# Kernel tuning notes

Measured on AMD Instinct MI355X. Metric: run time of the kernel, lower is better.

Reference implementation:

```python
import jax, jax.numpy as jnp
import numpy as np

N_NODES = 20000


def _agg(feat, src, dst):
    # copy_u + sum: for each edge, message = feat[src]; sum at dst over in-edges.
    # feat: [N, F], src/dst: [E] int32 -> [N, F]
    msgs = feat[src]  # [E, F]
    return jax.ops.segment_sum(msgs, dst, num_segments=N_NODES)


def setup_inputs() -> dict:
    key = jax.random.key(0)
    k1, k2, k3, k4, k5, k6, k7 = jax.random.split(key, 7)
    B, N, E = 4, N_NODES, 320000
    in_f, hid, out_f = 128, 256, 128
    features = jax.random.normal(k1, (B, N, in_f), dtype=jnp.float32)
    src = jax.random.randint(k2, (B, E), 0, N, dtype=jnp.int32)
    dst = jax.random.randint(k3, (B, E), 0, N, dtype=jnp.int32)
    s1 = 1.0 / np.sqrt(in_f)
    s2 = 1.0 / np.sqrt(hid)
    W1 = jax.random.uniform(k4, (in_f, hid), jnp.float32, -s1, s1)
    b1 = jax.random.uniform(k5, (hid,), jnp.float32, -s1, s1)
    W2 = jax.random.uniform(k6, (hid, out_f), jnp.float32, -s2, s2)
    b2 = jax.random.uniform(k7, (out_f,), jnp.float32, -s2, s2)
    return {"features": features, "src": src, "dst": dst,
            "W1": W1, "b1": b1, "W2": W2, "b2": b2}


def reference(features, src, dst, W1, b1, W2, b2):
    # vmap over the batch of graphs (replaces the per-graph Python loop)
    agg = jax.vmap(_agg)  # [B,N,F] -> [B,N,F]
    h = agg(features, src, dst)            # conv1 aggregation
    h = jnp.einsum('bnf,fh->bnh', h, W1) + b1  # conv1 linear
    h = jax.nn.relu(h)
    h = agg(h, src, dst)                   # conv2 aggregation
    out = jnp.einsum('bnh,ho->bno', h, W2) + b2  # conv2 linear
    return out
```

## Files before the change

kernel.cpp:

```cpp
#include <hip/hip_runtime.h>

#define NN 20000
#define NHALF 10000
#define NCH 16
#define SB 32
#define NBIN 625

typedef __attribute__((ext_vector_type(8))) __bf16 bf16x8;
typedef __attribute__((ext_vector_type(8))) unsigned short ushort8;
typedef __attribute__((ext_vector_type(4))) float f32x4;

__device__ __forceinline__ unsigned short f2bf(float f) {
    unsigned u = __builtin_bit_cast(unsigned, f);
    u += 0x7fff + ((u >> 16) & 1);
    return (unsigned short)(u >> 16);
}
__device__ __forceinline__ float bf2f(unsigned short h) {
    unsigned u = ((unsigned)h) << 16;
    return __builtin_bit_cast(float, u);
}


__global__ void k_tobf(const float* __restrict__ in, unsigned short* __restrict__ outp,
                       long n8) {
    long i = (long)blockIdx.x * 256 + threadIdx.x;
    if (i >= n8) return;
    const float4* s = (const float4*)(in + i * 8);
    float4 v0 = s[0], v1 = s[1];
    ushort8 r;
    r[0] = f2bf(v0.x); r[1] = f2bf(v0.y); r[2] = f2bf(v0.z); r[3] = f2bf(v0.w);
    r[4] = f2bf(v1.x); r[5] = f2bf(v1.y); r[6] = f2bf(v1.z); r[7] = f2bf(v1.w);
    *(ushort8*)(outp + i * 8) = r;
}


__global__ void k_hist(const int* __restrict__ dst, long dst_bs,
                       int* __restrict__ histc, int E, int ec) {
    int c = blockIdx.x, h = blockIdx.y, b = blockIdx.z;
    __shared__ int hist[NHALF];
    for (int i = threadIdx.x; i < NHALF; i += 1024) hist[i] = 0;
    __syncthreads();
    const int* d = dst + (size_t)b * dst_bs;
    int e0 = c * ec, e1 = min(e0 + ec, E);
    for (int e = e0 + threadIdx.x; e < e1; e += 1024) {
        int dd = d[e];
        if ((dd >= NHALF) == (h != 0)) atomicAdd(&hist[dd - h * NHALF], 1);
    }
    __syncthreads();
    int* out = histc + ((size_t)b * NCH + c) * NN + h * NHALF;
    for (int i = threadIdx.x; i < NHALF; i += 1024) out[i] = hist[i];
}


__global__ void k_scan2a(const int* __restrict__ histc,
                         int* __restrict__ offs, long off_bs,
                         int* __restrict__ chunkbase, int* __restrict__ btot) {
    int blk = blockIdx.x, b = blockIdx.z;
    const int* hc = histc + (size_t)b * NCH * NN;
    int* cb = chunkbase + (size_t)b * NCH * NN;
    int i = blk * NBIN + threadIdx.x;
    __shared__ int sums[1024];
    int hv[NCH];
    int s = 0;
    if (threadIdx.x < NBIN) {
#pragma unroll
        for (int c = 0; c < NCH; c++) { hv[c] = hc[c * NN + i]; s += hv[c]; }
    }
    sums[threadIdx.x] = (threadIdx.x < NBIN) ? s : 0;
    __syncthreads();
    for (int d2 = 1; d2 < 1024; d2 <<= 1) {
        int x = (threadIdx.x >= d2) ? sums[threadIdx.x - d2] : 0;
        __syncthreads();
        sums[threadIdx.x] += x;
        __syncthreads();
    }
    if (threadIdx.x == 1023) btot[b * 64 + blk] = sums[1023];
    if (threadIdx.x < NBIN) {
        int run = sums[threadIdx.x] - s;
        offs[(size_t)b * off_bs + i] = run;
#pragma unroll
        for (int c = 0; c < NCH; c++) { cb[c * NN + i] = run; run += hv[c]; }
    }
}


__global__ void k_scan2b(int* __restrict__ offs, long off_bs,
                         const int* __restrict__ btot, int* __restrict__ boff, int n) {
    int b = blockIdx.z;
    __shared__ int bo[SB + 1];
    int t = threadIdx.x;
    if (t == 0) {
        int run = 0;
        for (int k = 0; k < SB; k++) { bo[k] = run; run += btot[b * 64 + k]; }
        bo[SB] = run;
    }
    __syncthreads();
    if (t < SB) boff[b * 64 + t] = bo[t];
    if (t == 0) offs[(size_t)b * off_bs + n] = bo[SB];
    for (int i = t; i < n; i += 1024)
        offs[(size_t)b * off_bs + i] += bo[i / NBIN];
}


__global__ void k_fill2(const int* __restrict__ src, long src_bs,
                        const int* __restrict__ dst, long dst_bs,
                        const int* __restrict__ chunkbase,
                        const int* __restrict__ boff,
                        unsigned short* __restrict__ elist, long el_bs,
                        int E, int ec) {
    int c = blockIdx.x, h = blockIdx.y, b = blockIdx.z;
    __shared__ int cur[NHALF];
    __shared__ int bo[16];
    if (threadIdx.x < 16) bo[threadIdx.x] = boff[b * 64 + h * 16 + threadIdx.x];
    __syncthreads();
    const int* cb = chunkbase + ((size_t)b * NCH + c) * NN + h * NHALF;
    for (int i = threadIdx.x; i < NHALF; i += 1024)
        cur[i] = cb[i] + bo[i / NBIN];
    __syncthreads();
    const int* dp = dst + (size_t)b * dst_bs;
    const int* sp = src + (size_t)b * src_bs;
    unsigned short* el = elist + (size_t)b * el_bs;
    int e0 = c * ec, e1 = min(e0 + ec, E);
    for (int e = e0 + threadIdx.x; e < e1; e += 1024) {
        int dd = dp[e];
        if ((dd >= NHALF) == (h != 0)) {
            int p = atomicAdd(&cur[dd - h * NHALF], 1);
            el[p] = (unsigned short)sp[e];
        }
    }
}


template <bool BFOUT>
__global__ void k_agg(const unsigned short* __restrict__ feat, long feat_bs,
                      const int* __restrict__ offs, long off_bs,
                      const unsigned short* __restrict__ elist, long el_bs,
                      const float* __restrict__ bias,
                      void* __restrict__ o1,
                      long out_bs, int N, int nb, int nbx) {
    int gid = blockIdx.x;
    int xcd = gid & 7;
    int b = xcd % nb;
    int grp = xcd / nb;
    int pass = grp & 1;
    int sub = grp >> 1;
    int xh = (8 / nb) >> 1;
    int nbk = (gid >> 3) * xh + sub;
    if (nbk >= nbx) return;
    int g = threadIdx.x >> 3;
    int lane = threadIdx.x & 7;
    int n = nbk * 32 + g;
    if (n >= N) return;
    int col0 = pass * 64 + lane * 8;
    const unsigned short* fp = feat + (size_t)b * feat_bs + col0;
    const int* off = offs + (size_t)b * off_bs;
    const unsigned short* el = elist + (size_t)b * el_bs;
    int lo = off[n], hi = off[n + 1];
    float a0[8] = {}, a1[8] = {}, a2[8] = {}, a3[8] = {};
    auto acc = [&](float* a, ushort8 v) {
#pragma unroll
        for (int i = 0; i < 8; i++) a[i] += bf2f(v[i]);
    };
    int e = lo;
    for (; e < hi && (e & 3); e++)
        acc(a0, *(const ushort8*)&fp[(size_t)el[e] * 128]);
    for (; e + 4 <= hi; e += 4) {
        ushort4 idx = *(const ushort4*)&el[e];
        ushort8 v0 = *(const ushort8*)&fp[(size_t)idx.x * 128];
        ushort8 v1 = *(const ushort8*)&fp[(size_t)idx.y * 128];
        ushort8 v2 = *(const ushort8*)&fp[(size_t)idx.z * 128];
        ushort8 v3 = *(const ushort8*)&fp[(size_t)idx.w * 128];
        acc(a0, v0); acc(a1, v1); acc(a2, v2); acc(a3, v3);
    }
    for (; e < hi; e++)
        acc(a0, *(const ushort8*)&fp[(size_t)el[e] * 128]);
    float r[8];
#pragma unroll
    for (int i = 0; i < 8; i++) r[i] = (a0[i] + a1[i]) + (a2[i] + a3[i]);
    size_t oi = (size_t)b * out_bs + (size_t)n * 128 + col0;
    if (BFOUT) {
        ushort8 qh;
#pragma unroll
        for (int i = 0; i < 8; i++) qh[i] = f2bf(r[i]);
        *(ushort8*)((unsigned short*)o1 + oi) = qh;
    } else {
        float* op = (float*)o1 + oi;
        const float* bp = bias + col0;
#pragma unroll
        for (int i = 0; i < 8; i++) r[i] += bp[i];
        *(float4*)(op) = make_float4(r[0], r[1], r[2], r[3]);
        *(float4*)(op + 4) = make_float4(r[4], r[5], r[6], r[7]);
    }
}


__global__ void k_prep_w(const float* __restrict__ W1, const float* __restrict__ W2,
                         unsigned short* __restrict__ Wt1, unsigned short* __restrict__ Wt2) {
    int i = blockIdx.x * 256 + threadIdx.x;
    if (i < 128 * 256) {
        {
            int k = i / 256, n = i % 256;
            Wt1[n * 128 + k] = f2bf(W1[i]);
        }
        {
            int k = i / 128, n = i % 128;
            Wt2[n * 256 + k] = f2bf(W2[i]);
        }
    }
}


__launch_bounds__(256, 2)
__global__ void k_mlp(const unsigned short* __restrict__ A1, long A_bs,
                      const unsigned short* __restrict__ Wt1,
                      const unsigned short* __restrict__ Wt2,
                      const float* __restrict__ b1,
                      unsigned short* __restrict__ H2b, long C_bs,
                      int M, int ntiles) {
    __shared__ unsigned short HH[16 * 256];
    __shared__ unsigned short H2S[16 * 128];
    char* HHc = (char*)HH;
    char* H2c = (char*)H2S;
    int b = blockIdx.z;
    int w = threadIdx.x >> 6, lane = threadIdx.x & 63;
    int colg = lane & 15, kg = lane >> 4;

    bf16x8 w1f[4][4];
#pragma unroll
    for (int c = 0; c < 4; c++) {
        const unsigned short* ph = Wt1 + (size_t)(w * 64 + c * 16 + colg) * 128 + kg * 8;
#pragma unroll
        for (int ks = 0; ks < 4; ks++) w1f[c][ks] = *(const bf16x8*)(ph + ks * 32);
    }
    bf16x8 w2f[2][8];
#pragma unroll
    for (int c = 0; c < 2; c++) {
        const unsigned short* ph = Wt2 + (size_t)(w * 32 + c * 16 + colg) * 256 + kg * 8;
#pragma unroll
        for (int ks = 0; ks < 8; ks++) w2f[c][ks] = *(const bf16x8*)(ph + ks * 32);
    }
    float4 bv[4];
#pragma unroll
    for (int c = 0; c < 4; c++) bv[c] = *(const float4*)&b1[w * 64 + c * 16 + kg * 4];

    for (int t = blockIdx.x; t < ntiles; t += gridDim.x) {
        int row = t * 16 + colg;
        int rc = (row < M) ? row : M - 1;
        const unsigned short* pa = A1 + (size_t)b * A_bs + (size_t)rc * 128 + kg * 8;
        bf16x8 fa[4];
#pragma unroll
        for (int ks = 0; ks < 4; ks++) fa[ks] = *(const bf16x8*)(pa + ks * 32);

#pragma unroll
        for (int c = 0; c < 4; c++) {
            f32x4 a = (f32x4){0.f, 0.f, 0.f, 0.f};
#pragma unroll
            for (int ks = 0; ks < 4; ks++)
                a = __builtin_amdgcn_mfma_f32_16x16x32_bf16(w1f[c][ks], fa[ks], a, 0, 0, 0);
            float v[4] = {a[0] + bv[c].x, a[1] + bv[c].y, a[2] + bv[c].z, a[3] + bv[c].w};
#pragma unroll
            for (int j = 0; j < 4; j++) v[j] = fmaxf(v[j], 0.f);
            union { unsigned short u[4]; uint2 q; } qh;
#pragma unroll
            for (int j = 0; j < 4; j++) qh.u[j] = f2bf(v[j]);
            int off = (colg * 512 + w * 128 + c * 32 + kg * 8) ^ ((colg & 7) << 4);
            *(uint2*)(HHc + off) = qh.q;
        }
        __syncthreads();

        f32x4 a2[2];
        a2[0] = (f32x4){0.f, 0.f, 0.f, 0.f};
        a2[1] = (f32x4){0.f, 0.f, 0.f, 0.f};
#pragma unroll
        for (int ks2 = 0; ks2 < 8; ks2++) {
            int roff = (colg * 512 + ks2 * 64 + kg * 16) ^ ((colg & 7) << 4);
            bf16x8 fh = *(const bf16x8*)(HHc + roff);
            a2[0] = __builtin_amdgcn_mfma_f32_16x16x32_bf16(w2f[0][ks2], fh, a2[0], 0, 0, 0);
            a2[1] = __builtin_amdgcn_mfma_f32_16x16x32_bf16(w2f[1][ks2], fh, a2[1], 0, 0, 0);
        }
#pragma unroll
        for (int c = 0; c < 2; c++) {
            union { unsigned short u[4]; uint2 q; } qh;
#pragma unroll
            for (int j = 0; j < 4; j++) qh.u[j] = f2bf(a2[c][j]);
            int off = (colg * 256 + w * 64 + c * 32 + kg * 8) ^ ((colg & 7) << 4);
            *(uint2*)(H2c + off) = qh.q;
        }
        __syncthreads();

        {
            int idx = threadIdx.x;
            int r2 = idx >> 4;
            int u4 = idx & 15;
            int off = (r2 * 256 + u4 * 16) ^ ((r2 & 7) << 4);
            int grow = t * 16 + r2;
            if (grow < M) {
                uint4 v = *(const uint4*)(H2c + off);
                *(uint4*)(H2b + (size_t)b * C_bs + (size_t)grow * 128 + u4 * 8) = v;
            }
        }
    }
}


extern "C" void kernel_launch(void* const* d_in, const int* in_sizes, int n_in,
                              void* d_out, int out_size, void* d_ws, size_t ws_size,
                              hipStream_t stream) {
    const float* features = (const float*)d_in[0];
    const int* src = (const int*)d_in[1];
    const int* dst = (const int*)d_in[2];
    const float* W1 = (const float*)d_in[3];
    const float* b1 = (const float*)d_in[4];
    const float* W2 = (const float*)d_in[5];
    const float* b2 = (const float*)d_in[6];
    float* out = (float*)d_out;

    const int B = 4;
    const int N = NN;
    const int E = in_sizes[1] / B;

    auto need = [&](int nb) -> size_t {
        size_t bf = ((size_t)nb * N * (128 + 128 + 128)) * sizeof(unsigned short);
        size_t wt = 2 * 32768 * sizeof(unsigned short);
        size_t hist2 = 2 * (size_t)nb * NCH * N * sizeof(int);
        size_t ints = (size_t)nb * (size_t)(N + 1) * sizeof(int)
                    + (size_t)nb * E * sizeof(unsigned short)
                    + (size_t)nb * 128 * sizeof(int);
        return bf + wt + hist2 + ints + 256;
    };
    int nb = (ws_size >= need(4)) ? 4 : 1;
    int npass = B / nb;
    int xh = (8 / nb) >> 1;

    char* p = (char*)d_ws;
    unsigned short* fb  = (unsigned short*)p; p += (size_t)nb * N * 128 * sizeof(unsigned short);
    unsigned short* A1  = (unsigned short*)p; p += (size_t)nb * N * 128 * sizeof(unsigned short);
    unsigned short* H2b = (unsigned short*)p; p += (size_t)nb * N * 128 * sizeof(unsigned short);
    unsigned short* Wt1 = (unsigned short*)p; p += 32768 * sizeof(unsigned short);
    unsigned short* Wt2 = (unsigned short*)p; p += 32768 * sizeof(unsigned short);
    int* histc = (int*)p;     p += (size_t)nb * NCH * N * sizeof(int);
    int* chunkbase = (int*)p; p += (size_t)nb * NCH * N * sizeof(int);
    int* offs = (int*)p;      p += (size_t)nb * (N + 1) * sizeof(int);
    int* btot = (int*)p;      p += (size_t)nb * 64 * sizeof(int);
    int* boff = (int*)p;      p += (size_t)nb * 64 * sizeof(int);
    unsigned short* elist = (unsigned short*)p;

    k_prep_w<<<128, 256, 0, stream>>>(W1, W2, Wt1, Wt2);

    const int nbx = (N + 31) / 32;
    const int ntiles = (N + 15) / 16;
    const int ec = (E + NCH - 1) / NCH;
    dim3 gCsr(NCH, 2, nb);
    dim3 gAgg(8 * ((nbx + xh - 1) / xh), 1, 1);

    for (int pass = 0; pass < npass; pass++) {
        int b0 = pass * nb;
        const float* feat_p = features + (size_t)b0 * N * 128;
        const int* src_p = src + (size_t)b0 * E;
        const int* dst_p = dst + (size_t)b0 * E;
        float* out_p = out + (size_t)b0 * N * 128;

        long n8 = (long)nb * N * 128 / 8;
        k_tobf<<<(int)((n8 + 255) / 256), 256, 0, stream>>>(feat_p, fb, n8);

        k_hist<<<gCsr, 1024, 0, stream>>>(dst_p, E, histc, E, ec);
        k_scan2a<<<dim3(SB, 1, nb), 1024, 0, stream>>>(histc, offs, N + 1,
                                                       chunkbase, btot);
        k_scan2b<<<dim3(1, 1, nb), 1024, 0, stream>>>(offs, N + 1, btot, boff, N);
        k_fill2<<<gCsr, 1024, 0, stream>>>(src_p, E, dst_p, E, chunkbase, boff,
                                           elist, E, E, ec);

        k_agg<true><<<gAgg, 256, 0, stream>>>(fb, (long)N * 128, offs, N + 1,
                                              elist, E, nullptr, A1, (long)N * 128,
                                              N, nb, nbx);
        k_mlp<<<dim3(250, 1, nb), 256, 0, stream>>>(
            A1, (long)N * 128, Wt1, Wt2, b1, H2b, (long)N * 128, N, ntiles);
        k_agg<false><<<gAgg, 256, 0, stream>>>(H2b, (long)N * 128, offs, N + 1,
                                               elist, E, b2, out_p, (long)N * 128,
                                               N, nb, nbx);
    }
}
```

Before: 159.2 us.

## Fuse bf16 conversion, weight prep and histogram into one kernel; unroll gather by eight

Merges the feature-to-bf16 conversion, the weight transpose/convert and the destination histogram into a single launch, with the grid's y-dimension selecting the role, so they run concurrently and two launches are removed. The aggregation inner loop now issues eight independent gathered row loads per iteration instead of four, to expose more memory-level parallelism. The cost is more registers in the aggregation kernel and coarser conversion work: only 64 blocks, each with 1024 threads and a 10k-int shared histogram, now carry the dense feature conversion that used to be spread over many small blocks. Weight prep is repeated on every pass, but by default there is a single pass.

```diff
diff --git a/kernel.cpp b/kernel.cpp
--- a/kernel.cpp
+++ b/kernel.cpp
@@ -21,22 +21,42 @@
 }
 
 
-__global__ void k_tobf(const float* __restrict__ in, unsigned short* __restrict__ outp,
-                       long n8) {
-    long i = (long)blockIdx.x * 256 + threadIdx.x;
-    if (i >= n8) return;
-    const float4* s = (const float4*)(in + i * 8);
-    float4 v0 = s[0], v1 = s[1];
-    ushort8 r;
-    r[0] = f2bf(v0.x); r[1] = f2bf(v0.y); r[2] = f2bf(v0.z); r[3] = f2bf(v0.w);
-    r[4] = f2bf(v1.x); r[5] = f2bf(v1.y); r[6] = f2bf(v1.z); r[7] = f2bf(v1.w);
-    *(ushort8*)(outp + i * 8) = r;
-}
-
-
-__global__ void k_hist(const int* __restrict__ dst, long dst_bs,
-                       int* __restrict__ histc, int E, int ec) {
-    int c = blockIdx.x, h = blockIdx.y, b = blockIdx.z;
+__global__ void k_pre(const int* __restrict__ dst, long dst_bs,
+                      int* __restrict__ histc, int E, int ec,
+                      const float* __restrict__ feat, unsigned short* __restrict__ fb,
+                      const float* __restrict__ W1, const float* __restrict__ W2,
+                      unsigned short* __restrict__ Wt1, unsigned short* __restrict__ Wt2) {
+    int c = blockIdx.x, y = blockIdx.y, b = blockIdx.z;
+    if (y == 2) {
+        const int P = NN * 128 / 8 / NCH;
+        const float* fp = feat + (size_t)b * NN * 128;
+        unsigned short* op = fb + (size_t)b * NN * 128;
+        for (int i = c * P + threadIdx.x; i < (c + 1) * P; i += 1024) {
+            const float4* s = (const float4*)(fp + (size_t)i * 8);
+            float4 v0 = s[0], v1 = s[1];
+            ushort8 r;
+            r[0] = f2bf(v0.x); r[1] = f2bf(v0.y); r[2] = f2bf(v0.z); r[3] = f2bf(v0.w);
+            r[4] = f2bf(v1.x); r[5] = f2bf(v1.y); r[6] = f2bf(v1.z); r[7] = f2bf(v1.w);
+            *(ushort8*)(op + (size_t)i * 8) = r;
+        }
+        return;
+    }
+    if (y == 3) {
+        if (b == 0) {
+            for (int i = c * 2048 + threadIdx.x; i < (c + 1) * 2048; i += 1024) {
+                {
+                    int k = i / 256, n = i % 256;
+                    Wt1[n * 128 + k] = f2bf(W1[i]);
+                }
+                {
+                    int k = i / 128, n = i % 128;
+                    Wt2[n * 256 + k] = f2bf(W2[i]);
+                }
+            }
+        }
+        return;
+    }
+    int h = y;
     __shared__ int hist[NHALF];
     for (int i = threadIdx.x; i < NHALF; i += 1024) hist[i] = 0;
     __syncthreads();
@@ -83,7 +103,6 @@
     }
 }
 
-
 __global__ void k_scan2b(int* __restrict__ offs, long off_bs,
                          const int* __restrict__ btot, int* __restrict__ boff, int n) {
     int b = blockIdx.z;
@@ -100,7 +119,6 @@
     for (int i = t; i < n; i += 1024)
         offs[(size_t)b * off_bs + i] += bo[i / NBIN];
 }
-
 
 __global__ void k_fill2(const int* __restrict__ src, long src_bs,
                         const int* __restrict__ dst, long dst_bs,
@@ -164,13 +182,28 @@
     int e = lo;
     for (; e < hi && (e & 3); e++)
         acc(a0, *(const ushort8*)&fp[(size_t)el[e] * 128]);
-    for (; e + 4 <= hi; e += 4) {
-        ushort4 idx = *(const ushort4*)&el[e];
-        ushort8 v0 = *(const ushort8*)&fp[(size_t)idx.x * 128];
-        ushort8 v1 = *(const ushort8*)&fp[(size_t)idx.y * 128];
-        ushort8 v2 = *(const ushort8*)&fp[(size_t)idx.z * 128];
-        ushort8 v3 = *(const ushort8*)&fp[(size_t)idx.w * 128];
+    for (; e + 8 <= hi; e += 8) {
+        ushort4 i0 = *(const ushort4*)&el[e];
+        ushort4 i1 = *(const ushort4*)&el[e + 4];
+        ushort8 v0 = *(const ushort8*)&fp[(size_t)i0.x * 128];
+        ushort8 v1 = *(const ushort8*)&fp[(size_t)i0.y * 128];
+        ushort8 v2 = *(const ushort8*)&fp[(size_t)i0.z * 128];
+        ushort8 v3 = *(const ushort8*)&fp[(size_t)i0.w * 128];
+        ushort8 v4 = *(const ushort8*)&fp[(size_t)i1.x * 128];
+        ushort8 v5 = *(const ushort8*)&fp[(size_t)i1.y * 128];
+        ushort8 v6 = *(const ushort8*)&fp[(size_t)i1.z * 128];
+        ushort8 v7 = *(const ushort8*)&fp[(size_t)i1.w * 128];
         acc(a0, v0); acc(a1, v1); acc(a2, v2); acc(a3, v3);
+        acc(a0, v4); acc(a1, v5); acc(a2, v6); acc(a3, v7);
+    }
+    if (e + 4 <= hi) {
+        ushort4 i0 = *(const ushort4*)&el[e];
+        ushort8 v0 = *(const ushort8*)&fp[(size_t)i0.x * 128];
+        ushort8 v1 = *(const ushort8*)&fp[(size_t)i0.y * 128];
+        ushort8 v2 = *(const ushort8*)&fp[(size_t)i0.z * 128];
+        ushort8 v3 = *(const ushort8*)&fp[(size_t)i0.w * 128];
+        acc(a0, v0); acc(a1, v1); acc(a2, v2); acc(a3, v3);
+        e += 4;
     }
     for (; e < hi; e++)
         acc(a0, *(const ushort8*)&fp[(size_t)el[e] * 128]);
@@ -190,22 +223,6 @@
         for (int i = 0; i < 8; i++) r[i] += bp[i];
         *(float4*)(op) = make_float4(r[0], r[1], r[2], r[3]);
         *(float4*)(op + 4) = make_float4(r[4], r[5], r[6], r[7]);
-    }
-}
-
-
-__global__ void k_prep_w(const float* __restrict__ W1, const float* __restrict__ W2,
-                         unsigned short* __restrict__ Wt1, unsigned short* __restrict__ Wt2) {
-    int i = blockIdx.x * 256 + threadIdx.x;
-    if (i < 128 * 256) {
-        {
-            int k = i / 256, n = i % 256;
-            Wt1[n * 128 + k] = f2bf(W1[i]);
-        }
-        {
-            int k = i / 128, n = i % 128;
-            Wt2[n * 256 + k] = f2bf(W2[i]);
-        }
     }
 }
 
@@ -345,11 +362,10 @@
     int* boff = (int*)p;      p += (size_t)nb * 64 * sizeof(int);
     unsigned short* elist = (unsigned short*)p;
 
-    k_prep_w<<<128, 256, 0, stream>>>(W1, W2, Wt1, Wt2);
-
     const int nbx = (N + 31) / 32;
     const int ntiles = (N + 15) / 16;
     const int ec = (E + NCH - 1) / NCH;
+    dim3 gPre(NCH, 4, nb);
     dim3 gCsr(NCH, 2, nb);
     dim3 gAgg(8 * ((nbx + xh - 1) / xh), 1, 1);
 
@@ -360,10 +376,8 @@
         const int* dst_p = dst + (size_t)b0 * E;
         float* out_p = out + (size_t)b0 * N * 128;
 
-        long n8 = (long)nb * N * 128 / 8;
-        k_tobf<<<(int)((n8 + 255) / 256), 256, 0, stream>>>(feat_p, fb, n8);
-
-        k_hist<<<gCsr, 1024, 0, stream>>>(dst_p, E, histc, E, ec);
+        k_pre<<<gPre, 1024, 0, stream>>>(dst_p, E, histc, E, ec,
+                                         feat_p, fb, W1, W2, Wt1, Wt2);
         k_scan2a<<<dim3(SB, 1, nb), 1024, 0, stream>>>(histc, offs, N + 1,
                                                        chunkbase, btot);
         k_scan2b<<<dim3(1, 1, nb), 1024, 0, stream>>>(offs, N + 1, btot, boff, N);
```

New measurement: 151.0 us (median of 2 runs). 5.2% less time.
